# Optimization experiments

Hardware: AMD Instinct MI355X
Metric: run time of the kernel (lower is better)

## Reference

```python
import jax, jax.numpy as jnp
import numpy as np

# Axial permutations for num_dimensions=3, emb_dim=-1 (total rank 5), att_dims=[1,2,3]
PERMS = [[0, 2, 3, 1, 4], [0, 1, 3, 2, 4], [0, 1, 2, 3, 4]]
H_SELF = 8
H_CROSS = 8
E_HEAD = 64  # dims_embed[0] / (num_heads_self + num_heads_cross) = 1024/16


def layernorm(x, eps=1e-5):
    # nn.LayerNorm(elementwise_affine=False)
    m = x.mean(axis=-1, keepdims=True)
    v = x.var(axis=-1, keepdims=True)
    return (x - m) * jax.lax.rsqrt(v + eps)


def cross_attention(x, kv, wq, wkv, h, e):
    # x: [bb, t, d_q], kv: [bb, t_kv, d_kv]
    q = x @ wq                                   # [bb, t, h*e]
    k, v = jnp.split(kv @ wkv, 2, axis=-1)       # each [bb, t_kv, h*e]
    bb, t = q.shape[0], q.shape[1]
    tk = k.shape[1]
    q = q.reshape(bb, t, h, e)
    k = k.reshape(bb, tk, h, e)
    v = v.reshape(bb, tk, h, e)
    dots = jnp.einsum('bihe,bjhe->bhij', q, k) * (e ** -0.5)
    attn = jax.nn.softmax(dots, axis=-1)
    out = jnp.einsum('bhij,bjhe->bihe', attn, v)
    return out.reshape(bb, t, h * e)


def permute_to_from(x, kv, perm, wq, wkv, h, e):
    inv = list(np.argsort(perm))
    ax = jnp.transpose(x, perm)
    axkv = jnp.transpose(kv, perm)
    shape = list(ax.shape)
    shape_kv = list(axkv.shape)
    t, d = shape[-2], shape[-1]
    t_kv, d_kv = shape_kv[-2], shape_kv[-1]
    r1 = shape[1] / shape_kv[1]
    r2 = shape[2] / shape_kv[2]
    if int(r1) != 1:
        axkv = jnp.repeat(axkv, max(1, int(r1)), axis=1)
        ax = jnp.repeat(ax, max(1, int(1.0 / r1)), axis=1)
    if int(r2) != 1:
        axkv = jnp.repeat(axkv, max(1, int(r2)), axis=2)
        ax = jnp.repeat(ax, max(1, int(1.0 / r2)), axis=2)
    assert ax.shape[1:3] == axkv.shape[1:3]
    perm_shape = list(ax.shape)
    out = cross_attention(ax.reshape(-1, t, d), axkv.reshape(-1, t_kv, d_kv), wq, wkv, h, e)
    out = out.reshape(perm_shape[:-1] + [-1])
    if shape[1] < shape_kv[1]:  # field0 coarser along perm dim 1 -> mean-pool back
        out = out.reshape(shape[:2] + [int(1.0 / r1)] + perm_shape[2:-1] + [-1]).mean(axis=2)
    if shape[2] < shape_kv[2]:
        out = out.reshape(shape[:3] + [int(1.0 / r2)] + perm_shape[3:-1] + [-1]).mean(axis=3)
    out = out.reshape(shape[:-1] + [-1])
    return jnp.transpose(out, inv)


def setup_inputs() -> dict:
    key = jax.random.key(0)
    ks = jax.random.split(key, 8)
    B, T, LA, LO, D0, D1 = 32, 12, 12, 12, 1024, 512
    s = 0.02
    return {
        'x0': jax.random.normal(ks[0], (B, T, LA, LO, D0), dtype=jnp.float32),
        'x1': jax.random.normal(ks[1], (B, T, LA // 2, LO // 2, D1), dtype=jnp.float32),
        'wq_self': jax.random.normal(ks[2], (3, D0, 512), dtype=jnp.float32) * s,
        'wkv_self': jax.random.normal(ks[3], (3, D0, 1024), dtype=jnp.float32) * s,
        'wq_cross': jax.random.normal(ks[4], (3, D0, 512), dtype=jnp.float32) * s,
        'wkv_cross': jax.random.normal(ks[5], (3, D1, 1024), dtype=jnp.float32) * s,
        'w_out': jax.random.normal(ks[6], (3, 1024, D0), dtype=jnp.float32) * s,
        'b_out': jnp.zeros((3, D0), dtype=jnp.float32),
    }


def reference(x0, x1, wq_self, wkv_self, wq_cross, wkv_cross, w_out, b_out):
    pass_through = x0
    f0 = layernorm(x0)
    f1 = layernorm(x1)
    for ip, perm in enumerate(PERMS):
        o_self = permute_to_from(f0, f0, perm, wq_self[ip], wkv_self[ip], H_SELF, E_HEAD)
        o_cross = permute_to_from(f0, f1, perm, wq_cross[ip], wkv_cross[ip], H_CROSS, E_HEAD)
        f0 = jnp.concatenate([o_self, o_cross], axis=-1) @ w_out[ip] + b_out[ip]
    return pass_through + f0
```

## Files before the change

### kernel.cpp

```cpp
#include <hip/hip_runtime.h>
#include <hip/hip_bf16.h>


typedef __bf16 bf16x8 __attribute__((ext_vector_type(8)));
typedef float floatx4 __attribute__((ext_vector_type(4)));

#define N0 55296
#define N1 13824

#define RAW_BARRIER() asm volatile("s_barrier" ::: "memory")
#define VMCNT(n) asm volatile("s_waitcnt vmcnt(" #n ")" ::: "memory")

__device__ __forceinline__ void gload16(const void* g, void* l) {
    __builtin_amdgcn_global_load_lds(
        (const __attribute__((address_space(1))) unsigned int*)g,
        (__attribute__((address_space(3))) unsigned int*)l, 16, 0, 0);
}

template <int SIG>
__device__ __forceinline__ int mapRow(int i) {
    if (SIG == 0) return i;
    const int b = i / 1728, r = i % 1728;
    const int d1 = r / 144, r2 = r % 144, d2 = r2 / 12, d3 = r2 % 12;
    if (SIG == 1) return b * 1728 + d3 * 144 + d1 * 12 + d2;
    if (SIG == 2) return b * 1728 + d3 * 144 + d2 * 12 + d1;
    return b * 1728 + d1 * 144 + d3 * 12 + d2;
}

template <int D>
__device__ __forceinline__ void ln_body(const float* __restrict__ xr,
                                        __hip_bfloat16* __restrict__ yr)
{
    const int tid = threadIdx.x;
    float vals[D / 256];
    float s = 0.f, q = 0.f;
#pragma unroll
    for (int k = 0; k < D / 256; ++k) {
        float v = xr[tid + k * 256];
        vals[k] = v; s += v; q += v * v;
    }
#pragma unroll
    for (int off = 32; off > 0; off >>= 1) {
        s += __shfl_xor(s, off);
        q += __shfl_xor(q, off);
    }
    __shared__ float rs[4], rq[4];
    const int w = tid >> 6;
    if ((tid & 63) == 0) { rs[w] = s; rq[w] = q; }
    __syncthreads();
    s = rs[0] + rs[1] + rs[2] + rs[3];
    q = rq[0] + rq[1] + rq[2] + rq[3];
    const float mean = s * (1.f / D);
    const float var  = q * (1.f / D) - mean * mean;
    const float rstd = rsqrtf(var + 1e-5f);
#pragma unroll
    for (int k = 0; k < D / 256; ++k)
        yr[tid + k * 256] = __float2bfloat16((vals[k] - mean) * rstd);
}

__global__ __launch_bounds__(256)
void ln_all(const float* __restrict__ x0, const float* __restrict__ x1,
            __hip_bfloat16* __restrict__ f0, __hip_bfloat16* __restrict__ f1)
{
    const int row = blockIdx.x;
    if (row < N0) {
        ln_body<1024>(x0 + (size_t)row * 1024, f0 + (size_t)row * 1024);
    } else {
        const int r = row - N0;
        ln_body<512>(x1 + (size_t)r * 512, f1 + (size_t)r * 512);
    }
}

__global__ __launch_bounds__(256)
void transpose_all(const float* __restrict__ wqs, const float* __restrict__ wkvs,
                   const float* __restrict__ wqc, const float* __restrict__ wkvc,
                   const float* __restrict__ wo,
                   __hip_bfloat16* __restrict__ W1t,
                   __hip_bfloat16* __restrict__ W2t,
                   __hip_bfloat16* __restrict__ W3t)
{
    int idx = blockIdx.x;
    const float* src;
    __hip_bfloat16* dst;
    int K, N;
    if (idx < 1536) {
        const int ip = idx / 512; idx %= 512; K = 1024; N = 512;
        src = wqs + (size_t)ip * 524288;  dst = W1t + (size_t)ip * 2097152;
    } else if (idx < 4608) {
        idx -= 1536;
        const int ip = idx / 1024; idx %= 1024; K = 1024; N = 1024;
        src = wkvs + (size_t)ip * 1048576; dst = W1t + (size_t)ip * 2097152 + 524288;
    } else if (idx < 6144) {
        idx -= 4608;
        const int ip = idx / 512; idx %= 512; K = 1024; N = 512;
        src = wqc + (size_t)ip * 524288;  dst = W1t + (size_t)ip * 2097152 + 1572864;
    } else if (idx < 7680) {
        idx -= 6144;
        const int ip = idx / 512; idx %= 512; K = 512; N = 1024;
        src = wkvc + (size_t)ip * 524288; dst = W2t + (size_t)ip * 524288;
    } else {
        idx -= 7680;
        const int ip = idx / 1024; idx %= 1024; K = 1024; N = 1024;
        src = wo + (size_t)ip * 1048576;  dst = W3t + (size_t)ip * 1048576;
    }
    const int tiles_x = N >> 5;
    const int n0 = (idx % tiles_x) * 32, k0 = (idx / tiles_x) * 32;

    __shared__ float tile[32][33];
    const int tx = threadIdx.x & 31, ty = threadIdx.x >> 5;
#pragma unroll
    for (int d = 0; d < 4; ++d)
        tile[ty + d * 8][tx] = src[(size_t)(k0 + ty + d * 8) * N + n0 + tx];
    __syncthreads();
#pragma unroll
    for (int d = 0; d < 4; ++d)
        dst[(size_t)(n0 + ty + d * 8) * K + k0 + tx] = __float2bfloat16(tile[tx][ty + d * 8]);
}

__global__ __launch_bounds__(256)
void cast_w3o(const float* __restrict__ wo, __hip_bfloat16* __restrict__ W3o)
{
    const size_t i = ((size_t)blockIdx.x * 256 + threadIdx.x) * 4;
    const float4 v = *(const float4*)(wo + i);
    __hip_bfloat16 o[4] = { __float2bfloat16(v.x), __float2bfloat16(v.y),
                            __float2bfloat16(v.z), __float2bfloat16(v.w) };
    *(uint2*)(W3o + i) = *(const uint2*)o;
}

__global__ __launch_bounds__(256)
void bfold_kernel(const float* __restrict__ b_out,
                  const __hip_bfloat16* __restrict__ W1t,
                  float* __restrict__ bf)
{
    const int idx = blockIdx.x * 256 + threadIdx.x;
    const int j = idx >> 11, n = idx & 2047;
    const float* b = b_out + j * 1024;
    const __hip_bfloat16* w = W1t + ((size_t)(j + 1) * 2048 + n) * 1024;
    float s = 0.f;
#pragma unroll 4
    for (int d = 0; d < 1024; ++d) s += b[d] * __bfloat162float(w[d]);
    bf[idx] = s;
}

template <int EPI, int SIG>
__global__ __launch_bounds__(512)
void gemm8p(const __hip_bfloat16* __restrict__ A,
            const __hip_bfloat16* __restrict__ Bt,
            void* __restrict__ Cv,
            const float* __restrict__ bias,
            const float* __restrict__ resid,
            int M, int N, int K, int lda)
{
    __shared__ __align__(16) char lds[131072];

    const int gx  = gridDim.x;
    const int nwg = gx * gridDim.y;
    const int bid = blockIdx.y * gx + blockIdx.x;
    const int swz = (bid & 7) * (nwg >> 3) + (bid >> 3);
    const int m0 = (swz / gx) * 256;
    const int n0 = (swz % gx) * 256;

    const int t    = threadIdx.x;
    const int w    = t >> 6;
    const int lane = t & 63;
    const int wr   = w >> 2;
    const int wc   = w & 3;
    const int fr   = lane & 15;
    const int ksl  = lane >> 4;

    floatx4 acc[8][4] = {};

    const int tr   = t >> 3;
    const int scol = ((t & 7) ^ (tr & 7)) << 3;
    const __hip_bfloat16* aP[4];
#pragma unroll
    for (int r = 0; r < 4; ++r)
        aP[r] = A + (size_t)mapRow<SIG>(m0 + tr + r * 64) * lda + scol;
    const __hip_bfloat16* bG = Bt + (size_t)(n0 + ((tr >> 5) * 64) + (tr & 31)) * K + scol;
    const int ldst = t * 16;

    const int cg0 = ksl ^ (fr & 7);
    const int aO0 = (wr * 64 + fr) * 128 + cg0 * 16;
    const int bO0 = (wc * 32 + fr) * 128 + cg0 * 16;

    auto stageA = [&](char* buf, int h, int ka) {
        gload16(aP[h]     + ka, buf + h * 16384 + ldst);
        gload16(aP[h + 2] + ka, buf + h * 16384 + 8192 + ldst);
    };
    auto stageB = [&](char* buf, int h, int kb) {
        gload16(bG + kb + (size_t)(h * 32)       * K, buf + 32768 + h * 16384 + ldst);
        gload16(bG + kb + (size_t)(h * 32 + 128) * K, buf + 32768 + h * 16384 + 8192 + ldst);
    };

    const char* bufC = lds;
    auto ldA = [&](int h, bf16x8 (&a)[2][4]) {
#pragma unroll
        for (int mm = 0; mm < 4; ++mm) {
            a[0][mm] = *(const bf16x8*)(bufC + h * 16384 + mm * 2048 + aO0);
            a[1][mm] = *(const bf16x8*)(bufC + h * 16384 + mm * 2048 + (aO0 ^ 64));
        }
    };
    auto ldB = [&](int h, bf16x8 (&b)[2][2]) {
#pragma unroll
        for (int nn = 0; nn < 2; ++nn) {
            b[0][nn] = *(const bf16x8*)(bufC + 32768 + h * 16384 + nn * 2048 + bO0);
            b[1][nn] = *(const bf16x8*)(bufC + 32768 + h * 16384 + nn * 2048 + (bO0 ^ 64));
        }
    };
    auto quad = [&](bf16x8 (&a)[2][4], bf16x8 (&b)[2][2], int mlo, int nlo) {
        __builtin_amdgcn_s_setprio(1);
#pragma unroll
        for (int kk = 0; kk < 2; ++kk)
#pragma unroll
            for (int mm = 0; mm < 4; ++mm)
#pragma unroll
                for (int nn = 0; nn < 2; ++nn)
                    acc[mlo + mm][nlo + nn] = __builtin_amdgcn_mfma_f32_16x16x32_bf16(
                        a[kk][mm], b[kk][nn], acc[mlo + mm][nlo + nn], 0, 0, 0);
        __builtin_amdgcn_s_setprio(0);
    };

    const int NT = K >> 6;

    stageA(lds, 0, 0);
    stageB(lds, 0, 0);
    stageA(lds, 1, 0);
    stageB(lds, 1, 0);
    VMCNT(4);
    RAW_BARRIER();

    bf16x8 a0[2][4], a1[2][4], b0[2][2], b1[2][2];

    for (int tt = 0; tt < NT - 1; ++tt) {
        bufC = lds + ((tt & 1) << 16);
        char* bufN = lds + (((tt + 1) & 1) << 16);
        const int kc = (tt + 1) << 6;
        ldA(0, a0); ldB(0, b0);
        stageA(bufN, 0, kc);
        RAW_BARRIER(); __builtin_amdgcn_sched_barrier(0);
        quad(a0, b0, 0, 0);
        VMCNT(4); RAW_BARRIER();
        ldA(1, a1);
        stageB(bufN, 0, kc);
        RAW_BARRIER(); __builtin_amdgcn_sched_barrier(0);
        quad(a1, b0, 4, 0);
        VMCNT(4); RAW_BARRIER();
        ldB(1, b1);
        stageA(bufN, 1, kc);
        RAW_BARRIER(); __builtin_amdgcn_sched_barrier(0);
        quad(a0, b1, 0, 2);
        RAW_BARRIER();
        stageB(bufN, 1, kc);
        RAW_BARRIER(); __builtin_amdgcn_sched_barrier(0);
        quad(a1, b1, 4, 2);
        VMCNT(4); RAW_BARRIER();
    }

    bufC = lds + (((NT - 1) & 1) << 16);
    ldA(0, a0); ldB(0, b0);
    RAW_BARRIER(); __builtin_amdgcn_sched_barrier(0);
    quad(a0, b0, 0, 0);
    VMCNT(2); RAW_BARRIER();
    ldA(1, a1);
    RAW_BARRIER(); __builtin_amdgcn_sched_barrier(0);
    quad(a1, b0, 4, 0);
    VMCNT(0); RAW_BARRIER();
    ldB(1, b1);
    RAW_BARRIER(); __builtin_amdgcn_sched_barrier(0);
    quad(a0, b1, 0, 2);
    quad(a1, b1, 4, 2);

#pragma unroll
    for (int m = 0; m < 8; ++m) {
#pragma unroll
        for (int n = 0; n < 4; ++n) {
            const int col = n0 + wc * 64 + n * 16 + fr;
#pragma unroll
            for (int r = 0; r < 4; ++r) {
                const int row = m0 + wr * 128 + m * 16 + ksl * 4 + r;
                const size_t idx = (size_t)row * N + col;
                const float v = acc[m][n][r];
                if (EPI == 0) {
                    ((__hip_bfloat16*)Cv)[idx] = __float2bfloat16(v);
                } else if (EPI == 1) {
                    ((__hip_bfloat16*)Cv)[idx] = __float2bfloat16(v + bias[col]);
                } else {
                    ((float*)Cv)[idx] = resid[idx] + v + bias[col];
                }
            }
        }
    }
}

__global__ __launch_bounds__(512)
void attn_fused(const __hip_bfloat16* __restrict__ qkv,
                const __hip_bfloat16* __restrict__ kvc,
                __hip_bfloat16* __restrict__ out, int ip)
{
    __shared__ __align__(16) __hip_bfloat16 R[12][2052];
    __shared__ __align__(16) __hip_bfloat16 KV[12][1032];
    __shared__ __hip_bfloat16 P[16][12][12];

    const int g   = blockIdx.x;
    const int tid = threadIdx.x;

    const int b  = g / 144;
    const int u1 = (g / 12) % 12;
    const int u2 = g % 12;
    int kvb, kvstride, tkc;
    if (ip == 0) {
        kvb = b * 432 + (u1 >> 1) * 6 + (u2 >> 1); kvstride = 36; tkc = 12;
    } else if (ip == 1) {
        kvb = b * 432 + u1 * 36 + (u2 >> 1); kvstride = 6; tkc = 6;
    } else {
        kvb = b * 432 + u1 * 36 + (u2 >> 1) * 6; kvstride = 1; tkc = 6;
    }

    const uint4* src = (const uint4*)(qkv + (size_t)g * 12 * 2048);
    for (int idx = tid; idx < 12 * 256; idx += 512) {
        const int row = idx >> 8, cg = idx & 255;
        *(uint4*)(&R[row][cg * 8]) = src[row * 256 + cg];
    }
    for (int idx = tid; idx < tkc * 128; idx += 512) {
        const int row = idx >> 7, cg = idx & 127;
        const uint4* kvr = (const uint4*)(kvc + (size_t)(kvb + row * kvstride) * 3072);
        *(uint4*)(&KV[row][cg * 8]) = kvr[cg];
    }
    __syncthreads();

    const int nd_self = 8 * 12 * 12;
    const int nd = nd_self + 8 * 12 * tkc;
    for (int idx = tid; idx < nd; idx += 512) {
        int h, i, j;
        const __hip_bfloat162 *q2, *k2;
        bool self = idx < nd_self;
        if (self) {
            h = idx / 144; const int rem = idx % 144; i = rem / 12; j = rem % 12;
            q2 = (const __hip_bfloat162*)(&R[i][h * 64]);
            k2 = (const __hip_bfloat162*)(&R[j][512 + h * 64]);
        } else {
            const int x = idx - nd_self;
            h = x / (12 * tkc); const int rem = x % (12 * tkc); i = rem / tkc; j = rem % tkc;
            q2 = (const __hip_bfloat162*)(&R[i][1536 + h * 64]);
            k2 = (const __hip_bfloat162*)(&KV[j][h * 64]);
        }
        float s = 0.f;
#pragma unroll
        for (int e = 0; e < 32; ++e) {
            const float2 qf = __bfloat1622float2(q2[e]);
            const float2 kf = __bfloat1622float2(k2[e]);
            s += qf.x * kf.x + qf.y * kf.y;
        }
        P[self ? h : 8 + h][i][j] = __float2bfloat16(s * 0.125f);
    }
    __syncthreads();

    if (tid < 192) {
        const int half = tid / 96, h = (tid % 96) / 12, i = tid % 12;
        const int tk = half ? tkc : 12;
        __hip_bfloat16* p = &P[half * 8 + h][i][0];
        float v[12];
        float mx = -1e30f;
        for (int j = 0; j < tk; ++j) { v[j] = __bfloat162float(p[j]); mx = fmaxf(mx, v[j]); }
        float sum = 0.f;
        for (int j = 0; j < tk; ++j) { v[j] = __expf(v[j] - mx); sum += v[j]; }
        const float inv = 1.f / sum;
        for (int j = 0; j < tk; ++j) p[j] = __float2bfloat16(v[j] * inv);
    }
    __syncthreads();

    for (int idx = tid; idx < 12 * 512; idx += 512) {
        const int i = idx >> 9, c2 = idx & 511;
        const int col = c2 * 2;
        float a0 = 0.f, a1 = 0.f;
        if (c2 < 256) {
            const int h = col >> 6;
            for (int j = 0; j < 12; ++j) {
                const float p = __bfloat162float(P[h][i][j]);
                a0 += p * __bfloat162float(R[j][1024 + col]);
                a1 += p * __bfloat162float(R[j][1024 + col + 1]);
            }
        } else {
            const int cc = col - 512;
            const int h = cc >> 6;
            for (int j = 0; j < tkc; ++j) {
                const float p = __bfloat162float(P[8 + h][i][j]);
                a0 += p * __bfloat162float(KV[j][512 + cc]);
                a1 += p * __bfloat162float(KV[j][512 + cc + 1]);
            }
        }
        __hip_bfloat16 o[2] = { __float2bfloat16(a0), __float2bfloat16(a1) };
        *(uint*)(out + (size_t)(g * 12 + i) * 1024 + col) = *(const uint*)o;
    }
}

extern "C" void kernel_launch(void* const* d_in, const int* in_sizes, int n_in,
                              void* d_out, int out_size, void* d_ws, size_t ws_size,
                              hipStream_t stream)
{
    (void)in_sizes; (void)n_in; (void)out_size; (void)ws_size;
    const float* x0        = (const float*)d_in[0];
    const float* x1        = (const float*)d_in[1];
    const float* wq_self   = (const float*)d_in[2];
    const float* wkv_self  = (const float*)d_in[3];
    const float* wq_cross  = (const float*)d_in[4];
    const float* wkv_cross = (const float*)d_in[5];
    const float* w_out     = (const float*)d_in[6];
    const float* b_out     = (const float*)d_in[7];

    __hip_bfloat16* qkv = (__hip_bfloat16*)d_out;

    char* ws = (char*)d_ws;
    size_t off = 0;
    auto alloc = [&](size_t bytes) {
        void* p = ws + off;
        off += (bytes + 255) & ~(size_t)255;
        return p;
    };
    __hip_bfloat16* f0   = (__hip_bfloat16*)alloc((size_t)N0 * 1024 * 2);
    __hip_bfloat16* f1   = (__hip_bfloat16*)alloc((size_t)N1 * 512 * 2);
    __hip_bfloat16* kvc3 = (__hip_bfloat16*)alloc((size_t)N1 * 3072 * 2);
    __hip_bfloat16* W1t  = (__hip_bfloat16*)alloc((size_t)3 * 2048 * 1024 * 2);
    __hip_bfloat16* W2t  = (__hip_bfloat16*)alloc((size_t)3 * 1024 * 512 * 2);
    __hip_bfloat16* W3t  = (__hip_bfloat16*)alloc((size_t)3 * 1024 * 1024 * 2);
    __hip_bfloat16* W3o  = (__hip_bfloat16*)alloc((size_t)2 * 1024 * 1024 * 2);
    __hip_bfloat16* Wf   = (__hip_bfloat16*)alloc((size_t)2 * 2048 * 1024 * 2);
    float*          bfo  = (float*)alloc((size_t)2 * 2048 * 4);

    ln_all<<<N0 + N1, 256, 0, stream>>>(x0, x1, f0, f1);
    transpose_all<<<10752, 256, 0, stream>>>(wq_self, wkv_self, wq_cross,
                                             wkv_cross, w_out, W1t, W2t, W3t);
    cast_w3o<<<2048, 256, 0, stream>>>(w_out, W3o);
    bfold_kernel<<<16, 256, 0, stream>>>(b_out, W1t, bfo);
    for (int j = 0; j < 2; ++j)
        gemm8p<0, 0><<<dim3(4, 8), 512, 0, stream>>>(
            W1t + (size_t)(j + 1) * 2048 * 1024, W3o + (size_t)j * 1024 * 1024,
            Wf + (size_t)j * 2048 * 1024, nullptr, nullptr, 2048, 1024, 1024, 1024);
    gemm8p<0, 0><<<dim3(12, 54), 512, 0, stream>>>(
        f1, W2t, kvc3, nullptr, nullptr, N1, 3072, 512, 512);

    gemm8p<0, 1><<<dim3(8, 216), 512, 0, stream>>>(
        f0, W1t, qkv, nullptr, nullptr, N0, 2048, 1024, 1024);
    attn_fused<<<4608, 512, 0, stream>>>(qkv, kvc3, f0, 0);

    gemm8p<1, 2><<<dim3(8, 216), 512, 0, stream>>>(
        f0, Wf, qkv, bfo, nullptr, N0, 2048, 1024, 1024);
    attn_fused<<<4608, 512, 0, stream>>>(qkv, kvc3 + 1024, f0, 1);

    gemm8p<1, 3><<<dim3(8, 216), 512, 0, stream>>>(
        f0, Wf + (size_t)2048 * 1024, qkv, bfo + 2048, nullptr, N0, 2048, 1024, 1024);
    attn_fused<<<4608, 512, 0, stream>>>(qkv, kvc3 + 2048, f0, 2);

    gemm8p<2, 0><<<dim3(4, 216), 512, 0, stream>>>(
        f0, W3t + (size_t)2 * 1024 * 1024, d_out, b_out + 2 * 1024, x0,
        N0, 1024, 1024, 1024);
}
```

Before: 1.597 ms.

## Switch GEMM to 32x32x16 MFMA tiles and vectorize layernorm loads/stores

The GEMM inner kernel now uses 32x32x16 bf16 MFMA instructions with 16-element accumulators in place of 16x16x32. The LDS fragment addressing and the epilogue row/column mapping are rewritten to match. Larger MFMA tiles cut the instruction count and LDS fragment reads per FLOP, at the cost of a different swizzle pattern and a more scattered epilogue store layout. Layernorm also changes to vectorized float4/float2 loads and packed bf16 stores, which alters the per-thread element assignment.

```diff
diff --git a/kernel.cpp b/kernel.cpp
--- a/kernel.cpp
+++ b/kernel.cpp
@@ -4,6 +4,7 @@
 
 typedef __bf16 bf16x8 __attribute__((ext_vector_type(8)));
 typedef float floatx4 __attribute__((ext_vector_type(4)));
+typedef float floatx16 __attribute__((ext_vector_type(16)));
 
 #define N0 55296
 #define N1 13824
@@ -31,14 +32,19 @@
 __device__ __forceinline__ void ln_body(const float* __restrict__ xr,
                                         __hip_bfloat16* __restrict__ yr)
 {
+    constexpr int V = D / 256;
     const int tid = threadIdx.x;
-    float vals[D / 256];
+    float vals[V];
+    if constexpr (V == 4) {
+        const float4 t4 = *(const float4*)(xr + tid * 4);
+        vals[0] = t4.x; vals[1] = t4.y; vals[2] = t4.z; vals[3] = t4.w;
+    } else {
+        const float2 t2 = *(const float2*)(xr + tid * 2);
+        vals[0] = t2.x; vals[1] = t2.y;
+    }
     float s = 0.f, q = 0.f;
 #pragma unroll
-    for (int k = 0; k < D / 256; ++k) {
-        float v = xr[tid + k * 256];
-        vals[k] = v; s += v; q += v * v;
-    }
+    for (int k = 0; k < V; ++k) { s += vals[k]; q += vals[k] * vals[k]; }
 #pragma unroll
     for (int off = 32; off > 0; off >>= 1) {
         s += __shfl_xor(s, off);
@@ -53,9 +59,11 @@
     const float mean = s * (1.f / D);
     const float var  = q * (1.f / D) - mean * mean;
     const float rstd = rsqrtf(var + 1e-5f);
-#pragma unroll
-    for (int k = 0; k < D / 256; ++k)
-        yr[tid + k * 256] = __float2bfloat16((vals[k] - mean) * rstd);
+    __hip_bfloat16 o[V];
+#pragma unroll
+    for (int k = 0; k < V; ++k) o[k] = __float2bfloat16((vals[k] - mean) * rstd);
+    if constexpr (V == 4) *(uint2*)(yr + tid * 4) = *(const uint2*)o;
+    else                  *(uint*)(yr + tid * 2)  = *(const uint*)o;
 }
 
 __global__ __launch_bounds__(256)
@@ -165,10 +173,10 @@
     const int lane = t & 63;
     const int wr   = w >> 2;
     const int wc   = w & 3;
-    const int fr   = lane & 15;
-    const int ksl  = lane >> 4;
-
-    floatx4 acc[8][4] = {};
+    const int l31  = lane & 31;
+    const int kh   = lane >> 5;
+
+    floatx16 acc[4][2] = {};
 
     const int tr   = t >> 3;
     const int scol = ((t & 7) ^ (tr & 7)) << 3;
@@ -179,9 +187,9 @@
     const __hip_bfloat16* bG = Bt + (size_t)(n0 + ((tr >> 5) * 64) + (tr & 31)) * K + scol;
     const int ldst = t * 16;
 
-    const int cg0 = ksl ^ (fr & 7);
-    const int aO0 = (wr * 64 + fr) * 128 + cg0 * 16;
-    const int bO0 = (wc * 32 + fr) * 128 + cg0 * 16;
+    const int sw   = ((kh ^ (l31 & 7)) << 4);
+    const int aOfs = wr * 8192 + l31 * 128 + sw;
+    const int bOfs = 32768 + (wc * 32 + l31) * 128 + sw;
 
     auto stageA = [&](char* buf, int h, int ka) {
         gload16(aP[h]     + ka, buf + h * 16384 + ldst);
@@ -195,28 +203,24 @@
     const char* bufC = lds;
     auto ldA = [&](int h, bf16x8 (&a)[2][4]) {
 #pragma unroll
-        for (int mm = 0; mm < 4; ++mm) {
-            a[0][mm] = *(const bf16x8*)(bufC + h * 16384 + mm * 2048 + aO0);
-            a[1][mm] = *(const bf16x8*)(bufC + h * 16384 + mm * 2048 + (aO0 ^ 64));
-        }
-    };
-    auto ldB = [&](int h, bf16x8 (&b)[2][2]) {
-#pragma unroll
-        for (int nn = 0; nn < 2; ++nn) {
-            b[0][nn] = *(const bf16x8*)(bufC + 32768 + h * 16384 + nn * 2048 + bO0);
-            b[1][nn] = *(const bf16x8*)(bufC + 32768 + h * 16384 + nn * 2048 + (bO0 ^ 64));
-        }
-    };
-    auto quad = [&](bf16x8 (&a)[2][4], bf16x8 (&b)[2][2], int mlo, int nlo) {
+        for (int mf = 0; mf < 2; ++mf)
+#pragma unroll
+            for (int ks = 0; ks < 4; ++ks)
+                a[mf][ks] = *(const bf16x8*)(bufC + ((h * 16384 + mf * 4096 + aOfs) ^ (ks * 32)));
+    };
+    auto ldB = [&](int h, bf16x8 (&b)[4]) {
+#pragma unroll
+        for (int ks = 0; ks < 4; ++ks)
+            b[ks] = *(const bf16x8*)(bufC + ((h * 16384 + bOfs) ^ (ks * 32)));
+    };
+    auto quad = [&](bf16x8 (&a)[2][4], bf16x8 (&b)[4], int mbase, int nf) {
         __builtin_amdgcn_s_setprio(1);
 #pragma unroll
-        for (int kk = 0; kk < 2; ++kk)
-#pragma unroll
-            for (int mm = 0; mm < 4; ++mm)
-#pragma unroll
-                for (int nn = 0; nn < 2; ++nn)
-                    acc[mlo + mm][nlo + nn] = __builtin_amdgcn_mfma_f32_16x16x32_bf16(
-                        a[kk][mm], b[kk][nn], acc[mlo + mm][nlo + nn], 0, 0, 0);
+        for (int ks = 0; ks < 4; ++ks)
+#pragma unroll
+            for (int mf = 0; mf < 2; ++mf)
+                acc[mbase + mf][nf] = __builtin_amdgcn_mfma_f32_32x32x16_bf16(
+                    a[mf][ks], b[ks], acc[mbase + mf][nf], 0, 0, 0);
         __builtin_amdgcn_s_setprio(0);
     };
 
@@ -229,7 +233,7 @@
     VMCNT(4);
     RAW_BARRIER();
 
-    bf16x8 a0[2][4], a1[2][4], b0[2][2], b1[2][2];
+    bf16x8 a0[2][4], a1[2][4], b0[4], b1[4];
 
     for (int tt = 0; tt < NT - 1; ++tt) {
         bufC = lds + ((tt & 1) << 16);
@@ -243,16 +247,16 @@
         ldA(1, a1);
         stageB(bufN, 0, kc);
         RAW_BARRIER(); __builtin_amdgcn_sched_barrier(0);
-        quad(a1, b0, 4, 0);
+        quad(a1, b0, 2, 0);
         VMCNT(4); RAW_BARRIER();
         ldB(1, b1);
         stageA(bufN, 1, kc);
         RAW_BARRIER(); __builtin_amdgcn_sched_barrier(0);
-        quad(a0, b1, 0, 2);
+        quad(a0, b1, 0, 1);
         RAW_BARRIER();
         stageB(bufN, 1, kc);
         RAW_BARRIER(); __builtin_amdgcn_sched_barrier(0);
-        quad(a1, b1, 4, 2);
+        quad(a1, b1, 2, 1);
         VMCNT(4); RAW_BARRIER();
     }
 
@@ -263,23 +267,23 @@
     VMCNT(2); RAW_BARRIER();
     ldA(1, a1);
     RAW_BARRIER(); __builtin_amdgcn_sched_barrier(0);
-    quad(a1, b0, 4, 0);
+    quad(a1, b0, 2, 0);
     VMCNT(0); RAW_BARRIER();
     ldB(1, b1);
     RAW_BARRIER(); __builtin_amdgcn_sched_barrier(0);
-    quad(a0, b1, 0, 2);
-    quad(a1, b1, 4, 2);
-
-#pragma unroll
-    for (int m = 0; m < 8; ++m) {
-#pragma unroll
-        for (int n = 0; n < 4; ++n) {
-            const int col = n0 + wc * 64 + n * 16 + fr;
-#pragma unroll
-            for (int r = 0; r < 4; ++r) {
-                const int row = m0 + wr * 128 + m * 16 + ksl * 4 + r;
+    quad(a0, b1, 0, 1);
+    quad(a1, b1, 2, 1);
+
+#pragma unroll
+    for (int mf = 0; mf < 4; ++mf) {
+#pragma unroll
+        for (int nf = 0; nf < 2; ++nf) {
+            const int col = n0 + wc * 64 + nf * 32 + l31;
+#pragma unroll
+            for (int reg = 0; reg < 16; ++reg) {
+                const int row = m0 + wr * 128 + mf * 32 + (reg & 3) + ((reg >> 2) << 3) + (kh << 2);
                 const size_t idx = (size_t)row * N + col;
-                const float v = acc[m][n][r];
+                const float v = acc[mf][nf][reg];
                 if (EPI == 0) {
                     ((__hip_bfloat16*)Cv)[idx] = __float2bfloat16(v);
                 } else if (EPI == 1) {
```

After: 1.675 ms. 4.9% more time.
